# Performance work log

Measured on AMD Instinct MI355X. Metric: run time of the kernel, lower is better.

## Reference

```python
import jax, jax.numpy as jnp
import numpy as np

N = 100000      # nodes
E = 1600000     # edges (avg degree 16)
EMB = 128
L = 3           # num_layers
NUM_OPS = 64
MAX_BW = 64     # max_bitwidth
P = 4           # max_num_params


def setup_inputs() -> dict:
    key = jax.random.key(0)
    ks = jax.random.split(key, 24)
    w = lambda k, s: jax.random.normal(k, s, jnp.float32) * 0.05
    return {
        "ops": jax.random.randint(ks[0], (N,), 0, NUM_OPS),
        "params": jax.random.randint(ks[1], (N, P), 0, MAX_BW),
        "edge_src": jax.random.randint(ks[2], (E,), 0, N),
        "edge_dst": jax.random.randint(ks[3], (E,), 0, N),
        "op_emb_table": w(ks[4], (NUM_OPS, EMB)),
        "param_emb_table": w(ks[5], (MAX_BW, EMB)),
        "opmlp_w1": w(ks[6], ((1 + P) * EMB, EMB)), "opmlp_b1": w(ks[7], (EMB,)),
        "opmlp_w2": w(ks[8], (EMB, EMB)), "opmlp_b2": w(ks[9], (EMB,)),
        "conv_w": w(ks[10], (L, EMB, EMB)), "conv_b": w(ks[11], (L, EMB)),
        "mlp_w1": w(ks[12], (L * EMB, EMB)), "mlp_b1": w(ks[13], (EMB,)),
        "mlp_w2": w(ks[14], (EMB, EMB)), "mlp_b2": w(ks[15], (EMB,)),
        "mlpinv_w1": w(ks[16], (L * EMB, EMB)), "mlpinv_b1": w(ks[17], (EMB,)),
        "mlpinv_w2": w(ks[18], (EMB, EMB)), "mlpinv_b2": w(ks[19], (EMB,)),
        "comb_w": w(ks[20], (2 * EMB, EMB)), "comb_b": w(ks[21], (EMB,)),
    }


def _lrelu(x):
    return jax.nn.leaky_relu(x)  # slope 0.01, matches nn.LeakyReLU default


def _gin_mean(feat, src, dst, w, b):
    # DGL GINConv(aggregator='mean', eps=0): apply_func(feat + mean_in_neighbors(feat))
    n = feat.shape[0]
    msg = jax.ops.segment_sum(feat[src], dst, num_segments=n)           # [N, EMB]
    deg = jax.ops.segment_sum(jnp.ones(src.shape, feat.dtype), dst, num_segments=n)
    agg = msg / jnp.maximum(deg, 1.0)[:, None]
    return _lrelu((feat + agg) @ w + b)


def reference(ops, params, edge_src, edge_dst,
              op_emb_table, param_emb_table,
              opmlp_w1, opmlp_b1, opmlp_w2, opmlp_b2,
              conv_w, conv_b,
              mlp_w1, mlp_b1, mlp_w2, mlp_b2,
              mlpinv_w1, mlpinv_b1, mlpinv_w2, mlpinv_b2,
              comb_w, comb_b):
    n = ops.shape[0]
    # OpEmb: cat([op_emb] + per-param embs) -> MLP
    op_e = op_emb_table[ops]                               # [N, EMB]
    par_e = param_emb_table[params].reshape(n, -1)         # [N, P*EMB]
    h = jnp.concatenate([op_e, par_e], axis=1)
    h = _lrelu(h @ opmlp_w1 + opmlp_b1) @ opmlp_w2 + opmlp_b2
    states = h
    states_inv = h  # op_emb called twice on same inputs in the original

    conv_outs = []
    for i in range(L):
        states = _gin_mean(states, edge_src, edge_dst, conv_w[i], conv_b[i])
        conv_outs.append(states.sum(axis=0))
    final_sum = states.sum(axis=0)

    conv_outs_inv = []
    for i in range(L):
        states_inv = _gin_mean(states_inv, edge_dst, edge_src, conv_w[i], conv_b[i])
        # NOTE: original code appends states.sum(dim=0) (the final forward states),
        # not states_inv -- faithfully reproduced.
        conv_outs_inv.append(final_sum)

    g_emb = _lrelu(jnp.concatenate(conv_outs) @ mlp_w1 + mlp_b1) @ mlp_w2 + mlp_b2
    g_inv_emb = _lrelu(jnp.concatenate(conv_outs_inv) @ mlpinv_w1 + mlpinv_b1) @ mlpinv_w2 + mlpinv_b2

    out1 = jnp.concatenate([g_emb, g_inv_emb]) @ comb_w + comb_b          # [EMB]
    out2 = jnp.concatenate([states, states_inv], axis=1) @ comb_w + comb_b  # [N, EMB]
    return (out1, out2)
```

## Files before the change

kernel.cpp:

```cpp
#include <hip/hip_runtime.h>


typedef unsigned int  uint;
typedef unsigned short ushort;
typedef float  f32x4  __attribute__((ext_vector_type(4)));
typedef short  bf16x8 __attribute__((ext_vector_type(8)));

#define ABITS 9
#define CAPB  12288
#define CHUNK 2048

__device__ __forceinline__ float lrelu(float x) { return x > 0.0f ? x : 0.01f * x; }
__device__ __forceinline__ ushort f2b(float x) {
    uint u = __float_as_uint(x);
    return (ushort)((u + 0x7fffu + ((u >> 16) & 1u)) >> 16);
}
__device__ __forceinline__ float lof(uint u) { return __uint_as_float(u << 16); }
__device__ __forceinline__ float hif(uint u) { return __uint_as_float(u & 0xffff0000u); }

__global__ void tables_kernel(const float* __restrict__ opT, const float* __restrict__ parT,
                              const float* __restrict__ W1, float* __restrict__ A)
{
    int b = blockIdx.x;
    int t = b >> 6, v = b & 63, j = threadIdx.x;
    const float* emb = (t == 0 ? opT : parT) + v * 128;
    const float* w = W1 + (size_t)t * 128 * 128;
    float acc = 0.f;
    for (int k = 0; k < 128; ++k) acc += emb[k] * w[k * 128 + j];
    A[(size_t)b * 128 + j] = acc;
}

__global__ void prep_w(const float* __restrict__ convw, const float* __restrict__ ow2,
                       const float* __restrict__ cw, ushort* __restrict__ Wt)
{
    int t = blockIdx.x * 256 + threadIdx.x;
    int img = t >> 14, idx = t & 16383;
    int k = idx >> 7, c = idx & 127;
    const float* src;
    if (img < 3)      src = convw + img * 16384;
    else if (img == 3) src = ow2;
    else              src = cw + (img - 4) * 16384;
    float v = src[k * 128 + c];
    int byteoff = (img << 15) + (c << 8) + ((((k >> 3) ^ (c & 7)) << 4)) + ((k & 7) << 1);
    Wt[byteoff >> 1] = f2b(v);
}

__global__ __launch_bounds__(256) void binpass_kernel(
    const int* __restrict__ esrc, const int* __restrict__ edst, int E, int nb,
    int* __restrict__ gcur, uint2* __restrict__ binbuf)
{
    __shared__ int hist[448];
    __shared__ int lstart[448];
    __shared__ int gbase[448];
    __shared__ int lcur[448];
    __shared__ int gsum[8];
    __shared__ uint sKey[CHUNK * 2];
    __shared__ uint sPay[CHUNK * 2];
    __shared__ ushort sBin[CHUNK * 2];
    int tid = threadIdx.x, lane = tid & 63;
    int nb2 = nb * 2;

    for (int chunk = blockIdx.x; (size_t)chunk * CHUNK < (size_t)E; chunk += gridDim.x) {
        int base = chunk * CHUNK;
        int cnt = min(CHUNK, E - base);
        for (int i = tid; i < 448; i += 256) hist[i] = 0;
        __syncthreads();
        int s[8], d[8];
        #pragma unroll
        for (int i = 0; i < 8; ++i) {
            int idx = i * 256 + tid;
            if (idx < cnt) {
                s[i] = esrc[base + idx];
                d[i] = edst[base + idx];
                atomicAdd(&hist[d[i] >> ABITS], 1);
                atomicAdd(&hist[nb + (s[i] >> ABITS)], 1);
            } else s[i] = -1;
        }
        __syncthreads();
        #pragma unroll
        for (int k = 0; k < 2; ++k) {
            int idx = k * 256 + tid;
            int v = (idx < 448) ? hist[idx] : 0;
            int p = v;
            #pragma unroll
            for (int sh = 1; sh < 64; sh <<= 1) { int t = __shfl_up(p, sh, 64); if (lane >= sh) p += t; }
            if (idx < 448) {
                lstart[idx] = p - v;
                if (lane == 63) gsum[idx >> 6] = p;
            }
        }
        __syncthreads();
        if (tid == 0) { int run = 0; for (int g = 0; g < 7; ++g) { int t = gsum[g]; gsum[g] = run; run += t; } }
        __syncthreads();
        #pragma unroll
        for (int k = 0; k < 2; ++k) {
            int idx = k * 256 + tid;
            if (idx < 448) lstart[idx] += gsum[idx >> 6];
        }
        __syncthreads();
        for (int i = tid; i < nb2; i += 256) {
            int h = hist[i];
            gbase[i] = h ? atomicAdd(&gcur[i], h) : 0;
            lcur[i] = lstart[i];
        }
        __syncthreads();
        #pragma unroll
        for (int i = 0; i < 8; ++i) {
            if (s[i] >= 0) {
                int bf = d[i] >> ABITS;
                int p = atomicAdd(&lcur[bf], 1);
                sKey[p] = (uint)d[i]; sPay[p] = (uint)s[i]; sBin[p] = (ushort)bf;
                int bi = nb + (s[i] >> ABITS);
                int q = atomicAdd(&lcur[bi], 1);
                sKey[q] = (uint)s[i]; sPay[q] = (uint)d[i]; sBin[q] = (ushort)bi;
            }
        }
        __syncthreads();
        int total = 2 * cnt;
        for (int p = tid; p < total; p += 256) {
            int b = sBin[p];
            int pos = gbase[b] + (p - lstart[b]);
            if (pos < CAPB) binbuf[(size_t)b * CAPB + pos] = make_uint2(sKey[p], sPay[p]);
        }
        __syncthreads();
    }
}

__global__ __launch_bounds__(256) void csrpass_kernel(
    const uint2* __restrict__ binbuf, const int* __restrict__ gcur, int nb, int N,
    int* __restrict__ csr_f, int* __restrict__ off_f, int* __restrict__ cnt_f,
    int* __restrict__ csr_i, int* __restrict__ off_i, int* __restrict__ cnt_i)
{
    __shared__ int hist[512];
    __shared__ int loff[512];
    __shared__ int cur[512];
    __shared__ int gsum[8];
    int b = blockIdx.x;
    int dir = (b >= nb) ? 1 : 0;
    int binLocal = dir ? b - nb : b;
    int node0 = binLocal << ABITS;
    int nn = min(512, N - node0);
    int tid = threadIdx.x, lane = tid & 63;
    int total = min(gcur[b], CAPB);
    const uint2* seg = binbuf + (size_t)b * CAPB;
    int* csr = dir ? csr_i : csr_f;
    int* off = dir ? off_i : off_f;
    int* cnt = dir ? cnt_i : cnt_f;

    for (int i = tid; i < 512; i += 256) hist[i] = 0;
    __syncthreads();
    for (int e = tid; e < total; e += 256) {
        uint2 kp = seg[e];
        atomicAdd(&hist[kp.x - (uint)node0], 1);
    }
    __syncthreads();
    #pragma unroll
    for (int k = 0; k < 2; ++k) {
        int idx = k * 256 + tid;
        int v = hist[idx];
        int p = v;
        #pragma unroll
        for (int sh = 1; sh < 64; sh <<= 1) { int t = __shfl_up(p, sh, 64); if (lane >= sh) p += t; }
        loff[idx] = p - v;
        if (lane == 63) gsum[idx >> 6] = p;
    }
    __syncthreads();
    if (tid == 0) { int run = 0; for (int g = 0; g < 8; ++g) { int t = gsum[g]; gsum[g] = run; run += t; } }
    __syncthreads();
    #pragma unroll
    for (int k = 0; k < 2; ++k) {
        int idx = k * 256 + tid;
        loff[idx] += gsum[idx >> 6];
    }
    __syncthreads();
    int csrBase = binLocal * CAPB;
    for (int i = tid; i < 512; i += 256) {
        cur[i] = loff[i];
        if (i < nn) { off[node0 + i] = csrBase + loff[i]; cnt[node0 + i] = hist[i]; }
    }
    __syncthreads();
    int* csrSeg = csr + csrBase;
    for (int e = tid; e < total; e += 256) {
        uint2 kp = seg[e];
        int p = atomicAdd(&cur[kp.x - (uint)node0], 1);
        csrSeg[p] = (int)kp.y;
    }
}

__global__ __launch_bounds__(256, 8) void agg2_kernel(
    const ushort* __restrict__ Sf, const ushort* __restrict__ Si,
    const int* __restrict__ csr_f, const int* __restrict__ off_f, const int* __restrict__ cnt_f,
    const int* __restrict__ csr_i, const int* __restrict__ off_i, const int* __restrict__ cnt_i,
    ushort* __restrict__ msgf, ushort* __restrict__ msgi, int N)
{
    int gw = (blockIdx.x * 256 + threadIdx.x) >> 6;
    int lane = threadIdx.x & 63;
    int dir = 0, g = gw;
    if (g >= N) { dir = 1; g -= N; if (g >= N) return; }
    const uint* Sp = (const uint*)(dir ? Si : Sf);
    const int* csr = dir ? csr_i : csr_f;
    int off = (dir ? off_i : off_f)[g];
    int deg = (dir ? cnt_i : cnt_f)[g];

    float ax = 0.f, ay = 0.f;
    int d = 0;
    for (; d + 8 <= deg; d += 8) {
        int n0 = csr[off + d + 0], n1 = csr[off + d + 1];
        int n2 = csr[off + d + 2], n3 = csr[off + d + 3];
        int n4 = csr[off + d + 4], n5 = csr[off + d + 5];
        int n6 = csr[off + d + 6], n7 = csr[off + d + 7];
        uint v0 = Sp[(size_t)n0 * 64 + lane];
        uint v1 = Sp[(size_t)n1 * 64 + lane];
        uint v2 = Sp[(size_t)n2 * 64 + lane];
        uint v3 = Sp[(size_t)n3 * 64 + lane];
        uint v4 = Sp[(size_t)n4 * 64 + lane];
        uint v5 = Sp[(size_t)n5 * 64 + lane];
        uint v6 = Sp[(size_t)n6 * 64 + lane];
        uint v7 = Sp[(size_t)n7 * 64 + lane];
        ax += ((lof(v0) + lof(v1)) + (lof(v2) + lof(v3)))
            + ((lof(v4) + lof(v5)) + (lof(v6) + lof(v7)));
        ay += ((hif(v0) + hif(v1)) + (hif(v2) + hif(v3)))
            + ((hif(v4) + hif(v5)) + (hif(v6) + hif(v7)));
    }
    if (d + 4 <= deg) {
        int n0 = csr[off + d + 0], n1 = csr[off + d + 1];
        int n2 = csr[off + d + 2], n3 = csr[off + d + 3];
        uint v0 = Sp[(size_t)n0 * 64 + lane];
        uint v1 = Sp[(size_t)n1 * 64 + lane];
        uint v2 = Sp[(size_t)n2 * 64 + lane];
        uint v3 = Sp[(size_t)n3 * 64 + lane];
        ax += (lof(v0) + lof(v1)) + (lof(v2) + lof(v3));
        ay += (hif(v0) + hif(v1)) + (hif(v2) + hif(v3));
        d += 4;
    }
    for (; d < deg; ++d) {
        uint v = Sp[(size_t)csr[off + d] * 64 + lane];
        ax += lof(v); ay += hif(v);
    }
    float invd = 1.0f / fmaxf((float)deg, 1.0f);
    uint self = Sp[(size_t)g * 64 + lane];
    ax = lof(self) + ax * invd;
    ay = hif(self) + ay * invd;
    uint pk = (uint)f2b(ax) | ((uint)f2b(ay) << 16);
    ((uint*)(dir ? msgi : msgf))[(size_t)g * 64 + lane] = pk;
}

__device__ __forceinline__ void stage_w(const ushort* __restrict__ img, ushort* ldsW, int tid)
{
    const uint4* s = (const uint4*)img;
    uint4* d = (uint4*)ldsW;
    #pragma unroll
    for (int i = 0; i < 4; ++i) d[tid + (i << 9)] = s[tid + (i << 9)];
}

__global__ __launch_bounds__(512, 8) void gemm2_kernel(
    const ushort* __restrict__ msgf, const ushort* __restrict__ msgi,
    ushort* __restrict__ Sf_out, ushort* __restrict__ Si_out,
    const ushort* __restrict__ Wimg, const float* __restrict__ bias,
    float* __restrict__ colsum, int N)
{
    __shared__ __align__(16) ushort ldsW[16384];
    __shared__ float ldsCS[128];
    int tid = threadIdx.x, lane = tid & 63, w = tid >> 6;
    bool fwd = (blockIdx.x & 1) == 0;
    int node0 = (blockIdx.x >> 1) << 7;
    const ushort* msg = fwd ? msgf : msgi;
    ushort* Sout = fwd ? Sf_out : Si_out;

    stage_w(Wimg, ldsW, tid);
    if (fwd && tid < 128) ldsCS[tid] = 0.f;
    __syncthreads();

    int l15 = lane & 15, lg = lane >> 4;
    int node = node0 + (w << 4) + l15;
    int gr = min(node, N - 1);
    const char* Bb = (const char*)msg + ((size_t)gr << 8);

    f32x4 acc[8];
    #pragma unroll
    for (int i = 0; i < 8; ++i) acc[i] = f32x4{0.f, 0.f, 0.f, 0.f};
    #pragma unroll
    for (int kk = 0; kk < 4; ++kk) {
        bf16x8 bfr = *(const bf16x8*)(Bb + (((kk << 2) + lg) << 4));
        #pragma unroll
        for (int ct = 0; ct < 8; ++ct) {
            int c = (ct << 4) + l15;
            const char* Ab = (const char*)ldsW + c * 256;
            bf16x8 af = *(const bf16x8*)(Ab + ((((kk << 2) + lg) << 4) ^ ((c & 7) << 4)));
            acc[ct] = __builtin_amdgcn_mfma_f32_16x16x32_bf16(af, bfr, acc[ct], 0, 0, 0);
        }
    }

    bool valid = node < N;
    #pragma unroll
    for (int ct = 0; ct < 8; ++ct) {
        int ch0 = (ct << 4) + (lg << 2);
        float4 bb = *(const float4*)(bias + ch0);
        float o0 = lrelu(acc[ct][0] + bb.x);
        float o1 = lrelu(acc[ct][1] + bb.y);
        float o2 = lrelu(acc[ct][2] + bb.z);
        float o3 = lrelu(acc[ct][3] + bb.w);
        if (valid) {
            uint2 pk;
            pk.x = (uint)f2b(o0) | ((uint)f2b(o1) << 16);
            pk.y = (uint)f2b(o2) | ((uint)f2b(o3) << 16);
            *(uint2*)((char*)Sout + ((size_t)node << 8) + (ch0 << 1)) = pk;
        }
        if (fwd) {
            float c0 = valid ? o0 : 0.f, c1 = valid ? o1 : 0.f;
            float c2 = valid ? o2 : 0.f, c3 = valid ? o3 : 0.f;
            #pragma unroll
            for (int m = 1; m < 16; m <<= 1) {
                c0 += __shfl_xor(c0, m);
                c1 += __shfl_xor(c1, m);
                c2 += __shfl_xor(c2, m);
                c3 += __shfl_xor(c3, m);
            }
            if (l15 == 0) {
                atomicAdd(&ldsCS[ch0 + 0], c0);
                atomicAdd(&ldsCS[ch0 + 1], c1);
                atomicAdd(&ldsCS[ch0 + 2], c2);
                atomicAdd(&ldsCS[ch0 + 3], c3);
            }
        }
    }
    if (fwd) {
        __syncthreads();
        if (tid < 128) atomicAdd(&colsum[tid], ldsCS[tid]);
    }
}

__global__ __launch_bounds__(512, 4) void opemb_fused(
    const int* __restrict__ ops, const int* __restrict__ params,
    const float* __restrict__ Atab, const float* __restrict__ b1,
    const ushort* __restrict__ W2img, const float* __restrict__ b2,
    ushort* __restrict__ S0, int N)
{
    __shared__ __align__(16) ushort ldsW[16384];
    __shared__ __align__(16) ushort ldsA[16384];
    int tid = threadIdx.x, lane = tid & 63, w = tid >> 6;
    int node0 = blockIdx.x << 7;

    stage_w(W2img, ldsW, tid);

    int r = tid >> 2, sub = tid & 3;
    int g = node0 + r;
    float4 acc4[8];
    if (g < N) {
        int op = ops[g];
        const float4* T = (const float4*)(Atab + ((size_t)op << 7) + (sub << 5));
        #pragma unroll
        for (int q = 0; q < 8; ++q) acc4[q] = T[q];
        #pragma unroll
        for (int p = 0; p < 4; ++p) {
            int pv = params[(g << 2) + p];
            const float4* Tp = (const float4*)(Atab + ((size_t)((p + 1) * 64 + pv) << 7) + (sub << 5));
            #pragma unroll
            for (int q = 0; q < 8; ++q) {
                float4 u = Tp[q];
                acc4[q].x += u.x; acc4[q].y += u.y; acc4[q].z += u.z; acc4[q].w += u.w;
            }
        }
        const float4* Bv = (const float4*)(b1 + (sub << 5));
        #pragma unroll
        for (int q = 0; q < 8; ++q) {
            float4 bb = Bv[q];
            acc4[q].x = lrelu(acc4[q].x + bb.x);
            acc4[q].y = lrelu(acc4[q].y + bb.y);
            acc4[q].z = lrelu(acc4[q].z + bb.z);
            acc4[q].w = lrelu(acc4[q].w + bb.w);
        }
    } else {
        #pragma unroll
        for (int q = 0; q < 8; ++q) acc4[q] = make_float4(0.f, 0.f, 0.f, 0.f);
    }
    int akey = r & 7;
    #pragma unroll
    for (int q2 = 0; q2 < 4; ++q2) {
        int ch = (sub << 2) + q2;
        float4 a = acc4[q2 * 2], b = acc4[q2 * 2 + 1];
        uint4 pk;
        pk.x = (uint)f2b(a.x) | ((uint)f2b(a.y) << 16);
        pk.y = (uint)f2b(a.z) | ((uint)f2b(a.w) << 16);
        pk.z = (uint)f2b(b.x) | ((uint)f2b(b.y) << 16);
        pk.w = (uint)f2b(b.z) | ((uint)f2b(b.w) << 16);
        *(uint4*)((char*)ldsA + r * 256 + ((ch ^ akey) << 4)) = pk;
    }
    __syncthreads();

    int l15 = lane & 15, lg = lane >> 4;
    int node = node0 + (w << 4) + l15;
    int brow = (w << 4) + l15;
    const char* Bb = (const char*)ldsA + brow * 256;
    int bkey = (brow & 7) << 4;
    f32x4 acc[8];
    #pragma unroll
    for (int i = 0; i < 8; ++i) acc[i] = f32x4{0.f, 0.f, 0.f, 0.f};
    #pragma unroll
    for (int kk = 0; kk < 4; ++kk) {
        bf16x8 bfr = *(const bf16x8*)(Bb + ((((kk << 2) + lg) << 4) ^ bkey));
        #pragma unroll
        for (int ct = 0; ct < 8; ++ct) {
            int c = (ct << 4) + l15;
            const char* Ab = (const char*)ldsW + c * 256;
            bf16x8 af = *(const bf16x8*)(Ab + ((((kk << 2) + lg) << 4) ^ ((c & 7) << 4)));
            acc[ct] = __builtin_amdgcn_mfma_f32_16x16x32_bf16(af, bfr, acc[ct], 0, 0, 0);
        }
    }
    if (node < N) {
        #pragma unroll
        for (int ct = 0; ct < 8; ++ct) {
            int ch0 = (ct << 4) + (lg << 2);
            float4 bb = *(const float4*)(b2 + ch0);
            uint2 pk;
            pk.x = (uint)f2b(acc[ct][0] + bb.x) | ((uint)f2b(acc[ct][1] + bb.y) << 16);
            pk.y = (uint)f2b(acc[ct][2] + bb.z) | ((uint)f2b(acc[ct][3] + bb.w) << 16);
            *(uint2*)((char*)S0 + ((size_t)node << 8) + (ch0 << 1)) = pk;
        }
    }
}

__global__ __launch_bounds__(512, 8) void out2_fused(
    const ushort* __restrict__ Sf, const ushort* __restrict__ Si,
    const ushort* __restrict__ CWimg, const float* __restrict__ cb,
    float* __restrict__ out, int N)
{
    __shared__ __align__(16) ushort ldsW[16384];
    int tid = threadIdx.x, lane = tid & 63, w = tid >> 6;
    int node0 = blockIdx.x << 7;
    int l15 = lane & 15, lg = lane >> 4;
    int node = node0 + (w << 4) + l15;
    int gr = min(node, N - 1);
    f32x4 acc[8];
    #pragma unroll
    for (int i = 0; i < 8; ++i) acc[i] = f32x4{0.f, 0.f, 0.f, 0.f};
    #pragma unroll
    for (int pass = 0; pass < 2; ++pass) {
        if (pass) __syncthreads();
        stage_w(CWimg + (pass << 14), ldsW, tid);
        __syncthreads();
        const char* Bb = (const char*)(pass ? Si : Sf) + ((size_t)gr << 8);
        #pragma unroll
        for (int kk = 0; kk < 4; ++kk) {
            bf16x8 bfr = *(const bf16x8*)(Bb + (((kk << 2) + lg) << 4));
            #pragma unroll
            for (int ct = 0; ct < 8; ++ct) {
                int c = (ct << 4) + l15;
                const char* Ab = (const char*)ldsW + c * 256;
                bf16x8 af = *(const bf16x8*)(Ab + ((((kk << 2) + lg) << 4) ^ ((c & 7) << 4)));
                acc[ct] = __builtin_amdgcn_mfma_f32_16x16x32_bf16(af, bfr, acc[ct], 0, 0, 0);
            }
        }
    }
    if (node < N) {
        #pragma unroll
        for (int ct = 0; ct < 8; ++ct) {
            int ch0 = (ct << 4) + (lg << 2);
            float4 bb = *(const float4*)(cb + ch0);
            float4 o;
            o.x = acc[ct][0] + bb.x;
            o.y = acc[ct][1] + bb.y;
            o.z = acc[ct][2] + bb.z;
            o.w = acc[ct][3] + bb.w;
            *(float4*)(out + (size_t)node * 128 + ch0) = o;
        }
    }
}

__global__ void final_kernel(const float* __restrict__ convsum,
    const float* __restrict__ mw1, const float* __restrict__ mb1,
    const float* __restrict__ mw2, const float* __restrict__ mb2,
    const float* __restrict__ iw1, const float* __restrict__ ib1,
    const float* __restrict__ iw2, const float* __restrict__ ib2,
    const float* __restrict__ cw, const float* __restrict__ cb,
    float* __restrict__ out1)
{
    __shared__ float x[384];
    __shared__ float t1[128];
    __shared__ float t2[128];
    __shared__ float g1[128];
    __shared__ float g2[128];
    int j = threadIdx.x;
    x[j] = convsum[j]; x[128 + j] = convsum[128 + j]; x[256 + j] = convsum[256 + j];
    __syncthreads();
    float a = mb1[j];
    for (int k = 0; k < 384; ++k) a += x[k] * mw1[k * 128 + j];
    t1[j] = lrelu(a);
    float c = ib1[j];
    for (int k = 0; k < 384; ++k) c += x[256 + (k & 127)] * iw1[k * 128 + j];
    t2[j] = lrelu(c);
    __syncthreads();
    float b = mb2[j];
    float d = ib2[j];
    for (int k = 0; k < 128; ++k) {
        b += t1[k] * mw2[k * 128 + j];
        d += t2[k] * iw2[k * 128 + j];
    }
    g1[j] = b; g2[j] = d;
    __syncthreads();
    float e = cb[j];
    for (int k = 0; k < 128; ++k)
        e += g1[k] * cw[k * 128 + j] + g2[k] * cw[(128 + k) * 128 + j];
    out1[j] = e;
}

extern "C" void kernel_launch(void* const* d_in, const int* in_sizes, int n_in,
                              void* d_out, int out_size, void* d_ws, size_t ws_size,
                              hipStream_t stream)
{
    (void)n_in; (void)out_size; (void)ws_size;
    const int*   ops    = (const int*)d_in[0];
    const int*   params = (const int*)d_in[1];
    const int*   esrc   = (const int*)d_in[2];
    const int*   edst   = (const int*)d_in[3];
    const float* opT    = (const float*)d_in[4];
    const float* parT   = (const float*)d_in[5];
    const float* ow1    = (const float*)d_in[6];
    const float* ob1    = (const float*)d_in[7];
    const float* ow2    = (const float*)d_in[8];
    const float* ob2    = (const float*)d_in[9];
    const float* convw  = (const float*)d_in[10];
    const float* convb  = (const float*)d_in[11];
    const float* mw1    = (const float*)d_in[12];
    const float* mb1    = (const float*)d_in[13];
    const float* mw2    = (const float*)d_in[14];
    const float* mb2    = (const float*)d_in[15];
    const float* iw1    = (const float*)d_in[16];
    const float* ib1    = (const float*)d_in[17];
    const float* iw2    = (const float*)d_in[18];
    const float* ib2    = (const float*)d_in[19];
    const float* cw     = (const float*)d_in[20];
    const float* cb     = (const float*)d_in[21];

    const int N = in_sizes[0];
    const int E = in_sizes[2];
    const int nb = (N + 511) >> ABITS;
    const size_t NP = (size_t)N * 128;

    ushort* S0   = (ushort*)d_ws;
    ushort* S1   = S0 + NP;
    ushort* S2   = S1 + NP;
    ushort* S3   = S2 + NP;
    ushort* Wt   = S3 + NP;
    float*  Atab = (float*)(Wt + 6 * 16384);
    float*  convsum = Atab + 320 * 128;
    int*    gcur = (int*)(convsum + 512);
    uint2*  binbuf = (uint2*)(gcur + 512);
    int*    csr_f = (int*)(binbuf + (size_t)2 * nb * CAPB);
    int*    csr_i = csr_f + (size_t)nb * CAPB;
    int*    off_f = csr_i + (size_t)nb * CAPB;
    int*    cnt_f = off_f + N;
    int*    off_i = cnt_f + N;
    int*    cnt_i = off_i + N;

    float* out1 = (float*)d_out;
    float* out2 = out1 + 128;
    ushort* MSGF = (ushort*)out2;
    ushort* MSGI = MSGF + NP;

    hipMemsetAsync(convsum, 0, sizeof(float) * 1024, stream);

    tables_kernel<<<320, 128, 0, stream>>>(opT, parT, ow1, Atab);
    prep_w<<<384, 256, 0, stream>>>(convw, ow2, cw, Wt);
    binpass_kernel<<<(E + CHUNK - 1) / CHUNK, 256, 0, stream>>>(esrc, edst, E, nb, gcur, binbuf);
    csrpass_kernel<<<2 * nb, 256, 0, stream>>>(binbuf, gcur, nb, N,
                                               csr_f, off_f, cnt_f, csr_i, off_i, cnt_i);

    const int grid = (N + 127) / 128;
    opemb_fused<<<grid, 512, 0, stream>>>(ops, params, Atab, ob1, Wt + 3 * 16384, ob2, S0, N);

    const int aggGrid = (2 * N + 3) / 4;
    agg2_kernel<<<aggGrid, 256, 0, stream>>>(S0, S0, csr_f, off_f, cnt_f, csr_i, off_i, cnt_i, MSGF, MSGI, N);
    gemm2_kernel<<<2 * grid, 512, 0, stream>>>(MSGF, MSGI, S1, S3, Wt,             convb,       convsum,       N);
    agg2_kernel<<<aggGrid, 256, 0, stream>>>(S1, S3, csr_f, off_f, cnt_f, csr_i, off_i, cnt_i, MSGF, MSGI, N);
    gemm2_kernel<<<2 * grid, 512, 0, stream>>>(MSGF, MSGI, S0, S2, Wt + 16384,     convb + 128, convsum + 128, N);
    agg2_kernel<<<aggGrid, 256, 0, stream>>>(S0, S2, csr_f, off_f, cnt_f, csr_i, off_i, cnt_i, MSGF, MSGI, N);
    gemm2_kernel<<<2 * grid, 512, 0, stream>>>(MSGF, MSGI, S1, S3, Wt + 2 * 16384, convb + 256, convsum + 256, N);

    final_kernel<<<1, 128, 0, stream>>>(convsum, mw1, mb1, mw2, mb2,
                                        iw1, ib1, iw2, ib2, cw, cb, out1);
    out2_fused<<<grid, 512, 0, stream>>>(S1, S3, Wt + 4 * 16384, cb, out2, N);
}
```

Measured before the change: 687.4 us.

## Pre-scale CSR indices, split wave halves over neighbors, fuse final MLP into out2

CSR entries now store byte offsets (node<<8), so the gather needs no multiply. Each half-wave handles alternate neighbors and loads 8 bytes per lane, and the two halves are combined with a cross-half shuffle. The single-block final MLP kernel is folded into out2_fused as an extra block and parallelized across 512 threads, which removes one launch and its serial tail. The uint byte-offset math assumes N*256 fits in 32 bits, and the launch bound drops to 4 blocks per SM.

Result: no change. 675.4 us (-1.7%).

```diff
diff --git a/kernel.cpp b/kernel.cpp
--- a/kernel.cpp
+++ b/kernel.cpp
@@ -183,7 +183,7 @@
     for (int e = tid; e < total; e += 256) {
         uint2 kp = seg[e];
         int p = atomicAdd(&cur[kp.x - (uint)node0], 1);
-        csrSeg[p] = (int)kp.y;
+        csrSeg[p] = (int)(kp.y << 8);
     }
 }
 
@@ -197,52 +197,55 @@
     int lane = threadIdx.x & 63;
     int dir = 0, g = gw;
     if (g >= N) { dir = 1; g -= N; if (g >= N) return; }
-    const uint* Sp = (const uint*)(dir ? Si : Sf);
+    const char* Sp = (const char*)(dir ? Si : Sf);
     const int* csr = dir ? csr_i : csr_f;
     int off = (dir ? off_i : off_f)[g];
     int deg = (dir ? cnt_i : cnt_f)[g];
-
-    float ax = 0.f, ay = 0.f;
+    int half = lane >> 5;
+    int lb = (lane & 31) << 3;
+
+    float a0 = 0.f, a1 = 0.f, a2 = 0.f, a3 = 0.f;
     int d = 0;
     for (; d + 8 <= deg; d += 8) {
-        int n0 = csr[off + d + 0], n1 = csr[off + d + 1];
-        int n2 = csr[off + d + 2], n3 = csr[off + d + 3];
-        int n4 = csr[off + d + 4], n5 = csr[off + d + 5];
-        int n6 = csr[off + d + 6], n7 = csr[off + d + 7];
-        uint v0 = Sp[(size_t)n0 * 64 + lane];
-        uint v1 = Sp[(size_t)n1 * 64 + lane];
-        uint v2 = Sp[(size_t)n2 * 64 + lane];
-        uint v3 = Sp[(size_t)n3 * 64 + lane];
-        uint v4 = Sp[(size_t)n4 * 64 + lane];
-        uint v5 = Sp[(size_t)n5 * 64 + lane];
-        uint v6 = Sp[(size_t)n6 * 64 + lane];
-        uint v7 = Sp[(size_t)n7 * 64 + lane];
-        ax += ((lof(v0) + lof(v1)) + (lof(v2) + lof(v3)))
-            + ((lof(v4) + lof(v5)) + (lof(v6) + lof(v7)));
-        ay += ((hif(v0) + hif(v1)) + (hif(v2) + hif(v3)))
-            + ((hif(v4) + hif(v5)) + (hif(v6) + hif(v7)));
-    }
-    if (d + 4 <= deg) {
-        int n0 = csr[off + d + 0], n1 = csr[off + d + 1];
-        int n2 = csr[off + d + 2], n3 = csr[off + d + 3];
-        uint v0 = Sp[(size_t)n0 * 64 + lane];
-        uint v1 = Sp[(size_t)n1 * 64 + lane];
-        uint v2 = Sp[(size_t)n2 * 64 + lane];
-        uint v3 = Sp[(size_t)n3 * 64 + lane];
-        ax += (lof(v0) + lof(v1)) + (lof(v2) + lof(v3));
-        ay += (hif(v0) + hif(v1)) + (hif(v2) + hif(v3));
-        d += 4;
-    }
-    for (; d < deg; ++d) {
-        uint v = Sp[(size_t)csr[off + d] * 64 + lane];
-        ax += lof(v); ay += hif(v);
-    }
+        int b0 = csr[off + d + 0 + half];
+        int b1 = csr[off + d + 2 + half];
+        int b2 = csr[off + d + 4 + half];
+        int b3 = csr[off + d + 6 + half];
+        uint2 v0 = *(const uint2*)(Sp + (uint)(b0 + lb));
+        uint2 v1 = *(const uint2*)(Sp + (uint)(b1 + lb));
+        uint2 v2 = *(const uint2*)(Sp + (uint)(b2 + lb));
+        uint2 v3 = *(const uint2*)(Sp + (uint)(b3 + lb));
+        a0 += (lof(v0.x) + lof(v1.x)) + (lof(v2.x) + lof(v3.x));
+        a1 += (hif(v0.x) + hif(v1.x)) + (hif(v2.x) + hif(v3.x));
+        a2 += (lof(v0.y) + lof(v1.y)) + (lof(v2.y) + lof(v3.y));
+        a3 += (hif(v0.y) + hif(v1.y)) + (hif(v2.y) + hif(v3.y));
+    }
+    for (; d + 2 <= deg; d += 2) {
+        int b = csr[off + d + half];
+        uint2 v = *(const uint2*)(Sp + (uint)(b + lb));
+        a0 += lof(v.x); a1 += hif(v.x); a2 += lof(v.y); a3 += hif(v.y);
+    }
+    if (d < deg && half == 0) {
+        int b = csr[off + d];
+        uint2 v = *(const uint2*)(Sp + (uint)(b + lb));
+        a0 += lof(v.x); a1 += hif(v.x); a2 += lof(v.y); a3 += hif(v.y);
+    }
+    a0 += __shfl_xor(a0, 32);
+    a1 += __shfl_xor(a1, 32);
+    a2 += __shfl_xor(a2, 32);
+    a3 += __shfl_xor(a3, 32);
     float invd = 1.0f / fmaxf((float)deg, 1.0f);
-    uint self = Sp[(size_t)g * 64 + lane];
-    ax = lof(self) + ax * invd;
-    ay = hif(self) + ay * invd;
-    uint pk = (uint)f2b(ax) | ((uint)f2b(ay) << 16);
-    ((uint*)(dir ? msgi : msgf))[(size_t)g * 64 + lane] = pk;
+    uint2 self = *(const uint2*)(Sp + ((size_t)g << 8) + lb);
+    a0 = lof(self.x) + a0 * invd;
+    a1 = hif(self.x) + a1 * invd;
+    a2 = lof(self.y) + a2 * invd;
+    a3 = hif(self.y) + a3 * invd;
+    if (half == 0) {
+        uint2 pk;
+        pk.x = (uint)f2b(a0) | ((uint)f2b(a1) << 16);
+        pk.y = (uint)f2b(a2) | ((uint)f2b(a3) << 16);
+        *(uint2*)((char*)(dir ? msgi : msgf) + ((size_t)g << 8) + lb) = pk;
+    }
 }
 
 __device__ __forceinline__ void stage_w(const ushort* __restrict__ img, ushort* ldsW, int tid)
@@ -420,13 +423,73 @@
     }
 }
 
-__global__ __launch_bounds__(512, 8) void out2_fused(
+__device__ __forceinline__ void final_body(
+    float* lds, const float* __restrict__ convsum,
+    const float* __restrict__ mw1, const float* __restrict__ mb1,
+    const float* __restrict__ mw2, const float* __restrict__ mb2,
+    const float* __restrict__ iw1, const float* __restrict__ ib1,
+    const float* __restrict__ iw2, const float* __restrict__ ib2,
+    const float* __restrict__ cw, const float* __restrict__ cb,
+    float* __restrict__ out1)
+{
+    float* x  = lds;
+    float* pa = lds + 384;
+    float* pb = lds + 896;
+    float* t1 = lds + 1408;
+    float* t2 = lds + 1536;
+    int tid = threadIdx.x, j = tid & 127, s = tid >> 7;
+    if (tid < 384) x[tid] = convsum[tid];
+    __syncthreads();
+    float a = 0.f, c = 0.f;
+    for (int k = s * 96; k < s * 96 + 96; ++k) {
+        a += x[k] * mw1[k * 128 + j];
+        c += x[256 + (k & 127)] * iw1[k * 128 + j];
+    }
+    pa[tid] = a; pb[tid] = c;
+    __syncthreads();
+    if (s == 0) {
+        t1[j] = lrelu(pa[j] + pa[128 + j] + pa[256 + j] + pa[384 + j] + mb1[j]);
+        t2[j] = lrelu(pb[j] + pb[128 + j] + pb[256 + j] + pb[384 + j] + ib1[j]);
+    }
+    __syncthreads();
+    float b = 0.f, d = 0.f;
+    for (int k = s * 32; k < s * 32 + 32; ++k) {
+        b += t1[k] * mw2[k * 128 + j];
+        d += t2[k] * iw2[k * 128 + j];
+    }
+    pa[tid] = b; pb[tid] = d;
+    __syncthreads();
+    if (s == 0) {
+        t1[j] = pa[j] + pa[128 + j] + pa[256 + j] + pa[384 + j] + mb2[j];
+        t2[j] = pb[j] + pb[128 + j] + pb[256 + j] + pb[384 + j] + ib2[j];
+    }
+    __syncthreads();
+    float e = 0.f;
+    for (int k = s * 32; k < s * 32 + 32; ++k)
+        e += t1[k] * cw[k * 128 + j] + t2[k] * cw[(128 + k) * 128 + j];
+    pa[tid] = e;
+    __syncthreads();
+    if (s == 0) out1[j] = pa[j] + pa[128 + j] + pa[256 + j] + pa[384 + j] + cb[j];
+}
+
+__global__ __launch_bounds__(512, 4) void out2_fused(
     const ushort* __restrict__ Sf, const ushort* __restrict__ Si,
     const ushort* __restrict__ CWimg, const float* __restrict__ cb,
-    float* __restrict__ out, int N)
+    float* __restrict__ out, int gemmBlocks, int N,
+    const float* __restrict__ convsum,
+    const float* __restrict__ mw1, const float* __restrict__ mb1,
+    const float* __restrict__ mw2, const float* __restrict__ mb2,
+    const float* __restrict__ iw1, const float* __restrict__ ib1,
+    const float* __restrict__ iw2, const float* __restrict__ ib2,
+    const float* __restrict__ cw, float* __restrict__ out1)
 {
     __shared__ __align__(16) ushort ldsW[16384];
     int tid = threadIdx.x, lane = tid & 63, w = tid >> 6;
+    if ((int)blockIdx.x >= gemmBlocks) {
+        final_body((float*)ldsW, convsum, mw1, mb1, mw2, mb2,
+                   iw1, ib1, iw2, ib2, cw, cb, out1);
+        return;
+    }
     int node0 = blockIdx.x << 7;
     int l15 = lane & 15, lg = lane >> 4;
     int node = node0 + (w << 4) + l15;
@@ -465,43 +528,6 @@
             *(float4*)(out + (size_t)node * 128 + ch0) = o;
         }
     }
-}
-
-__global__ void final_kernel(const float* __restrict__ convsum,
-    const float* __restrict__ mw1, const float* __restrict__ mb1,
-    const float* __restrict__ mw2, const float* __restrict__ mb2,
-    const float* __restrict__ iw1, const float* __restrict__ ib1,
-    const float* __restrict__ iw2, const float* __restrict__ ib2,
-    const float* __restrict__ cw, const float* __restrict__ cb,
-    float* __restrict__ out1)
-{
-    __shared__ float x[384];
-    __shared__ float t1[128];
-    __shared__ float t2[128];
-    __shared__ float g1[128];
-    __shared__ float g2[128];
-    int j = threadIdx.x;
-    x[j] = convsum[j]; x[128 + j] = convsum[128 + j]; x[256 + j] = convsum[256 + j];
-    __syncthreads();
-    float a = mb1[j];
-    for (int k = 0; k < 384; ++k) a += x[k] * mw1[k * 128 + j];
-    t1[j] = lrelu(a);
-    float c = ib1[j];
-    for (int k = 0; k < 384; ++k) c += x[256 + (k & 127)] * iw1[k * 128 + j];
-    t2[j] = lrelu(c);
-    __syncthreads();
-    float b = mb2[j];
-    float d = ib2[j];
-    for (int k = 0; k < 128; ++k) {
-        b += t1[k] * mw2[k * 128 + j];
-        d += t2[k] * iw2[k * 128 + j];
-    }
-    g1[j] = b; g2[j] = d;
-    __syncthreads();
-    float e = cb[j];
-    for (int k = 0; k < 128; ++k)
-        e += g1[k] * cw[k * 128 + j] + g2[k] * cw[(128 + k) * 128 + j];
-    out1[j] = e;
 }
 
 extern "C" void kernel_launch(void* const* d_in, const int* in_sizes, int n_in,
@@ -577,7 +603,7 @@
     agg2_kernel<<<aggGrid, 256, 0, stream>>>(S0, S2, csr_f, off_f, cnt_f, csr_i, off_i, cnt_i, MSGF, MSGI, N);
     gemm2_kernel<<<2 * grid, 512, 0, stream>>>(MSGF, MSGI, S1, S3, Wt + 2 * 16384, convb + 256, convsum + 256, N);
 
-    final_kernel<<<1, 128, 0, stream>>>(convsum, mw1, mb1, mw2, mb2,
-                                        iw1, ib1, iw2, ib2, cw, cb, out1);
-    out2_fused<<<grid, 512, 0, stream>>>(S1, S3, Wt + 4 * 16384, cb, out2, N);
-}
+    out2_fused<<<grid + 1, 512, 0, stream>>>(S1, S3, Wt + 4 * 16384, cb, out2, grid, N,
+                                             convsum, mw1, mb1, mw2, mb2,
+                                             iw1, ib1, iw2, ib2, cw, out1);
+}
```
